# Kernel tuning notes

Hardware: AMD Instinct MI355X
Metric: run time of the kernel (lower is better)

Reference implementation:

```python
import jax, jax.numpy as jnp
import numpy as np

B, S, H = 1, 2048, 2048
QL, KVL = 1536, 512
NH, NOPE, ROPE, VD = 16, 128, 64, 128
IH, ID = 16, 128
TOPK = 512
EPS = 1e-6


def _rms_norm(x, g):
    return x * jax.lax.rsqrt(jnp.mean(x * x, -1, keepdims=True) + EPS) * g


def _layer_norm(x, g, b):
    m = jnp.mean(x, -1, keepdims=True)
    v = jnp.mean((x - m) ** 2, -1, keepdims=True)
    return (x - m) * jax.lax.rsqrt(v + EPS) * g + b


def _rope(x, cos, sin):
    # x: [B,S,h,D] (D even), cos/sin: [S,D//2]; neox-style rotate-halves
    x1, x2 = jnp.split(x, 2, -1)
    c = cos[None, :, None, :]
    s = sin[None, :, None, :]
    return jnp.concatenate([x1 * c - x2 * s, x1 * s + x2 * c], -1)


def setup_inputs() -> dict:
    key = jax.random.key(0)
    ks = jax.random.split(key, 10)
    rn = lambda k, sh: (jax.random.normal(k, sh) * 0.02).astype(jnp.float32)
    pos = jnp.arange(S, dtype=jnp.float32)
    inv = 1.0 / (10000.0 ** (jnp.arange(0, ROPE, 2, dtype=jnp.float32) / ROPE))
    ang = pos[:, None] * inv[None, :]  # [S, ROPE//2]
    return {
        "hidden_states": jax.random.normal(ks[0], (B, S, H), jnp.float32),
        "cos": jnp.cos(ang),
        "sin": jnp.sin(ang),
        "Wq_a": rn(ks[1], (H, QL)),
        "q_a_gamma": jnp.ones((QL,), jnp.float32),
        "Wq_b": rn(ks[2], (QL, NH * (NOPE + ROPE))),
        "Wkv_a": rn(ks[3], (H, KVL + ROPE)),
        "kv_a_gamma": jnp.ones((KVL,), jnp.float32),
        "Wkv_b": rn(ks[4], (KVL, NH * (NOPE + VD))),
        "Wo": rn(ks[5], (NH * VD, H)),
        "Wq_idx": rn(ks[6], (QL, IH * ID)),
        "Wk_idx": rn(ks[7], (H, ID)),
        "Ww_idx": rn(ks[8], (H, IH)),
        "kn_gamma": jnp.ones((ID,), jnp.float32),
        "kn_beta": jnp.zeros((ID,), jnp.float32),
        "topk": TOPK,
    }


def reference(hidden_states, cos, sin, Wq_a, q_a_gamma, Wq_b, Wkv_a, kv_a_gamma,
              Wkv_b, Wo, Wq_idx, Wk_idx, Ww_idx, kn_gamma, kn_beta, topk):
    b, s, _ = hidden_states.shape
    softmax_scale = (NOPE + ROPE) ** -0.5

    # ---- low-rank Q path ----
    q_a = _rms_norm(hidden_states @ Wq_a, q_a_gamma)                 # [B,S,QL]
    q = (q_a @ Wq_b).reshape(b, s, NH, NOPE + ROPE)
    q_nope, q_pe = q[..., :NOPE], _rope(q[..., NOPE:], cos, sin)

    # ---- latent KV path (MQA rope key) ----
    kv = hidden_states @ Wkv_a                                        # [B,S,KVL+ROPE]
    kv_c = _rms_norm(kv[..., :KVL], kv_a_gamma)
    k_pe = _rope(kv[..., KVL:][:, :, None, :], cos, sin)[:, :, 0]     # [B,S,ROPE]
    kvb = (kv_c @ Wkv_b).reshape(b, s, NH, NOPE + VD)
    k_nope, v = kvb[..., :NOPE], kvb[..., NOPE:]

    # ---- lightning indexer: I[t,s] = sum_h w[t,h] * relu(q_idx[t,h] . k_idx[s]) ----
    qi = (q_a @ Wq_idx).reshape(b, s, IH, ID)
    qi = jnp.concatenate([_rope(qi[..., :ROPE], cos, sin), qi[..., ROPE:]], -1)
    ki = _layer_norm(hidden_states @ Wk_idx, kn_gamma, kn_beta)       # [B,S,ID]
    ki = jnp.concatenate([_rope(ki[:, :, None, :ROPE], cos, sin)[:, :, 0], ki[..., ROPE:]], -1)
    w = hidden_states @ Ww_idx                                        # [B,S,IH]
    s_h = jax.nn.relu(jnp.einsum('bthd,bsd->bhts', qi, ki)) * (ID ** -0.5)
    idx_scores = jnp.einsum('bth,bhts->bts', w, s_h)                  # [B,S,S]

    causal = jnp.tril(jnp.ones((s, s), bool))
    idx_scores = jnp.where(causal[None], idx_scores, -jnp.inf)
    top_idx = jax.lax.top_k(idx_scores, topk)[1]                      # [B,S,topk]
    sel = jnp.zeros((b, s, s), bool).at[
        jnp.arange(b)[:, None, None], jnp.arange(s)[None, :, None], top_idx
    ].set(True)
    mask = sel & causal[None]                                         # [B,S,S]

    # ---- sparse MLA attention over selected tokens ----
    scores = (jnp.einsum('bthd,bshd->bhts', q_nope, k_nope)
              + jnp.einsum('bthd,bsd->bhts', q_pe, k_pe)) * softmax_scale
    scores = jnp.where(mask[:, None], scores, -jnp.inf)
    attn = jax.nn.softmax(scores, -1)                                 # [B,NH,S,S]
    out = jnp.einsum('bhts,bshd->bthd', attn, v).reshape(b, s, NH * VD)
    return out @ Wo                                                   # [B,S,H]
```

## Files before the change

kernel.cpp:

```cpp
#include <hip/hip_runtime.h>
#include <cstdint>
#include <cstddef>
#include <cmath>

typedef unsigned long long u64;
typedef __attribute__((ext_vector_type(8))) short bf16x8;
typedef __attribute__((ext_vector_type(4))) float f32x4;

static constexpr int S_    = 2048;
static constexpr int H_    = 2048;
static constexpr int TOPKC = 512;

#define SCALE_ATTN 0.07216878364870323f
#define ISCALE_ID  0.08838834764831845f
#define EPS_F 1e-6f

__device__ inline unsigned short f2b(float f) {
  unsigned u = __float_as_uint(f);
  return (unsigned short)((u + 0x7FFFu + ((u >> 16) & 1u)) >> 16);
}
__device__ inline float b2f(unsigned short b) {
  return __uint_as_float(((unsigned)b) << 16);
}
__device__ inline void gload16(const unsigned short* g, unsigned short* l) {
  __builtin_amdgcn_global_load_lds((const __attribute__((address_space(1))) void*)g,
                                   (__attribute__((address_space(3))) void*)l, 16, 0, 0);
}

__global__ __launch_bounds__(256) void k_gemm_bf16(
    const unsigned short* __restrict__ A, int lda,
    const unsigned short* __restrict__ Bt, int K,
    void* __restrict__ C, int ldc, int N, int out_bf16) {
  __shared__ unsigned short As[128 * 64];
  __shared__ unsigned short Bs[128 * 64];
  const int bm = blockIdx.y * 128, bn = blockIdx.x * 128;
  const int tid = threadIdx.x;
  const int lane = tid & 63, w = tid >> 6;
  const int wm = w >> 1, wn = w & 1;
  const int l15 = lane & 15, quarter = lane >> 4;
  const int srow = (lane >> 3), scol = (lane & 7) * 8;

  f32x4 acc[4][4];
#pragma unroll
  for (int i = 0; i < 4; i++)
#pragma unroll
    for (int j = 0; j < 4; j++) acc[i][j] = (f32x4){0.f, 0.f, 0.f, 0.f};

  for (int k0 = 0; k0 < K; k0 += 64) {
    __syncthreads();
#pragma unroll
    for (int i = 0; i < 4; i++) {
      int r0 = w * 32 + i * 8;
      gload16(A  + (size_t)(bm + r0 + srow) * lda + k0 + scol, &As[r0 * 64]);
      gload16(Bt + (size_t)(bn + r0 + srow) * K   + k0 + scol, &Bs[r0 * 64]);
    }
    __syncthreads();
#pragma unroll
    for (int kc = 0; kc < 2; kc++) {
      bf16x8 af[4], bfr[4];
#pragma unroll
      for (int mf = 0; mf < 4; mf++)
        af[mf] = *(const bf16x8*)(As + (wm * 64 + mf * 16 + l15) * 64 + kc * 32 + quarter * 8);
#pragma unroll
      for (int nf = 0; nf < 4; nf++)
        bfr[nf] = *(const bf16x8*)(Bs + (wn * 64 + nf * 16 + l15) * 64 + kc * 32 + quarter * 8);
#pragma unroll
      for (int mf = 0; mf < 4; mf++)
#pragma unroll
        for (int nf = 0; nf < 4; nf++)
          acc[mf][nf] = __builtin_amdgcn_mfma_f32_16x16x32_bf16(af[mf], bfr[nf], acc[mf][nf], 0, 0, 0);
    }
  }
#pragma unroll
  for (int mf = 0; mf < 4; mf++)
#pragma unroll
    for (int nf = 0; nf < 4; nf++)
#pragma unroll
      for (int r = 0; r < 4; r++) {
        int grow = bm + wm * 64 + mf * 16 + quarter * 4 + r;
        int gcol = bn + wn * 64 + nf * 16 + l15;
        if (gcol < N) {
          if (out_bf16) ((unsigned short*)C)[(size_t)grow * ldc + gcol] = f2b(acc[mf][nf][r]);
          else          ((float*)C)[(size_t)grow * ldc + gcol] = acc[mf][nf][r];
        }
      }
}

__device__ inline void tcast_tile(const float* __restrict__ W, int K, int N,
                                  unsigned short* __restrict__ dst,
                                  int r, int ntx, int tid, float (*T)[33]) {
  int xt = r % ntx, kt = r / ntx;
  int n0 = xt * 32, k0 = kt * 32;
#pragma unroll
  for (int i = 0; i < 4; i++) {
    int idx = tid + 256 * i;
    int rr = idx >> 5, c = idx & 31;
    T[rr][c] = W[(size_t)(k0 + rr) * N + n0 + c];
  }
  __syncthreads();
#pragma unroll
  for (int i = 0; i < 4; i++) {
    int idx = tid + 256 * i;
    int rr = idx >> 5, c = idx & 31;
    dst[(size_t)(n0 + rr) * K + k0 + c] = f2b(T[c][rr]);
  }
}

__global__ __launch_bounds__(256) void k_tcast_p1(
    const float* __restrict__ Wq_a, const float* __restrict__ Wkv_a,
    const float* __restrict__ Wk_idx, const float* __restrict__ Ww_idx,
    unsigned short* __restrict__ WT) {
  __shared__ float T[32][33];
  int bid = blockIdx.x, tid = threadIdx.x;
  if (bid < 3072)      tcast_tile(Wq_a,  2048, 1536, WT,                          bid,        48, tid, T);
  else if (bid < 4224) tcast_tile(Wkv_a, 2048,  576, WT + (size_t)1536 * 2048,    bid - 3072, 18, tid, T);
  else if (bid < 4480) tcast_tile(Wk_idx,2048,  128, WT + (size_t)2112 * 2048,    bid - 4224,  4, tid, T);
  else {
    int idx = (bid - 4480) * 256 + tid;
    int k = idx >> 4, n = idx & 15;
    WT[(size_t)(2240 + n) * 2048 + k] = f2b(Ww_idx[(size_t)k * 16 + n]);
  }
}

__global__ __launch_bounds__(256) void k_tcast_p2(
    const float* __restrict__ Wq_b, const float* __restrict__ Wq_idx,
    unsigned short* __restrict__ WT) {
  __shared__ float T[32][33];
  int bid = blockIdx.x, tid = threadIdx.x;
  if (bid < 4608) tcast_tile(Wq_b,   1536, 3072, WT,                        bid,        96, tid, T);
  else            tcast_tile(Wq_idx, 1536, 2048, WT + (size_t)3072 * 1536,  bid - 4608, 64, tid, T);
}

__global__ __launch_bounds__(256) void k_tcast_p3(
    const float* __restrict__ Wkv_b, const float* __restrict__ Wo,
    unsigned short* __restrict__ WT) {
  __shared__ float T[32][33];
  int bid = blockIdx.x, tid = threadIdx.x;
  if (bid < 2048) tcast_tile(Wkv_b,  512, 4096, WT,                       bid,        128, tid, T);
  else            tcast_tile(Wo,    2048, 2048, WT + (size_t)4096 * 512,  bid - 2048,  64, tid, T);
}

__global__ __launch_bounds__(256) void k_cast_bf16(const float* __restrict__ in, int pin,
                                                   unsigned short* __restrict__ outp, int pout,
                                                   int rows, int cols) {
  int cols4 = cols >> 2;
  int idx = blockIdx.x * 256 + threadIdx.x;
  if (idx >= rows * cols4) return;
  int r = idx / cols4, c = (idx - r * cols4) * 4;
  const float* ip = in + (size_t)r * pin + c;
  unsigned short* op = outp + (size_t)r * pout + c;
  op[0] = f2b(ip[0]); op[1] = f2b(ip[1]); op[2] = f2b(ip[2]); op[3] = f2b(ip[3]);
}

__global__ __launch_bounds__(256) void k_norms(
    const float* __restrict__ fat, int stride,
    const float* __restrict__ qg, const float* __restrict__ kvg,
    const float* __restrict__ kng, const float* __restrict__ knb,
    const float* __restrict__ cosb, const float* __restrict__ sinb,
    unsigned short* __restrict__ qa_b, unsigned short* __restrict__ kvc_b,
    unsigned short* __restrict__ kpe_b, unsigned short* __restrict__ ki_b) {
  int t = blockIdx.x, tid = threadIdx.x;
  const float* p = fat + (size_t)t * stride;
  __shared__ float red[256];
  __shared__ float buf[128];
  float x[6]; float s = 0.f;
#pragma unroll
  for (int i = 0; i < 6; i++) { x[i] = p[tid + 256 * i]; s += x[i] * x[i]; }
  red[tid] = s; __syncthreads();
  for (int st = 128; st > 0; st >>= 1) { if (tid < st) red[tid] += red[tid + st]; __syncthreads(); }
  float scl = rsqrtf(red[0] * (1.f / 1536.f) + EPS_F);
#pragma unroll
  for (int i = 0; i < 6; i++)
    qa_b[(size_t)t * 1536 + tid + 256 * i] = f2b(x[i] * scl * qg[tid + 256 * i]);
  __syncthreads();
  float y0 = p[1536 + tid], y1 = p[1792 + tid];
  red[tid] = y0 * y0 + y1 * y1; __syncthreads();
  for (int st = 128; st > 0; st >>= 1) { if (tid < st) red[tid] += red[tid + st]; __syncthreads(); }
  float scl2 = rsqrtf(red[0] * (1.f / 512.f) + EPS_F);
  kvc_b[(size_t)t * 512 + tid]       = f2b(y0 * scl2 * kvg[tid]);
  kvc_b[(size_t)t * 512 + 256 + tid] = f2b(y1 * scl2 * kvg[256 + tid]);
  if (tid < 32) {
    float a = p[2048 + tid], b = p[2080 + tid];
    float c = cosb[t * 32 + tid], sn = sinb[t * 32 + tid];
    kpe_b[(size_t)t * 64 + tid]      = f2b(a * c - b * sn);
    kpe_b[(size_t)t * 64 + 32 + tid] = f2b(a * sn + b * c);
  }
  __syncthreads();
  float z = (tid < 128) ? p[2112 + tid] : 0.f;
  red[tid] = z; __syncthreads();
  for (int st = 128; st > 0; st >>= 1) { if (tid < st) red[tid] += red[tid + st]; __syncthreads(); }
  float mean = red[0] * (1.f / 128.f);
  __syncthreads();
  float d = (tid < 128) ? (z - mean) : 0.f;
  red[tid] = d * d; __syncthreads();
  for (int st = 128; st > 0; st >>= 1) { if (tid < st) red[tid] += red[tid + st]; __syncthreads(); }
  float var = red[0] * (1.f / 128.f);
  if (tid < 128) buf[tid] = d * rsqrtf(var + EPS_F) * kng[tid] + knb[tid];
  __syncthreads();
  if (tid < 128) {
    float outv;
    if (tid < 32) {
      float c = cosb[t * 32 + tid], sn = sinb[t * 32 + tid];
      outv = buf[tid] * c - buf[tid + 32] * sn;
    } else if (tid < 64) {
      int j = tid - 32;
      float c = cosb[t * 32 + j], sn = sinb[t * 32 + j];
      outv = buf[j] * sn + buf[tid] * c;
    } else outv = buf[tid];
    ki_b[(size_t)t * 128 + tid] = f2b(outv);
  }
}

__global__ __launch_bounds__(256) void k_rope_b(unsigned short* __restrict__ base, int rowstride, int nh,
                                                int hstride, int off, const float* __restrict__ cosb,
                                                const float* __restrict__ sinb, int total) {
  int idx = blockIdx.x * 256 + threadIdx.x;
  if (idx >= total) return;
  int i = idx & 31, h = (idx >> 5) % nh, t = idx / (32 * nh);
  unsigned short* p = base + (size_t)t * rowstride + h * hstride + off;
  float x1 = b2f(p[i]), x2 = b2f(p[i + 32]);
  float c = cosb[t * 32 + i], s = sinb[t * 32 + i];
  p[i] = f2b(x1 * c - x2 * s);
  p[i + 32] = f2b(x1 * s + x2 * c);
}

__global__ __launch_bounds__(256) void k_idx_mfma(
    const unsigned short* __restrict__ qi_b, int qpitch,
    const unsigned short* __restrict__ ki_b,
    const float* __restrict__ wb, int wstride,
    float* __restrict__ out) {
  int bid = blockIdx.x;
  int tb = (int)((sqrtf(8.f * bid + 1.f) - 1.f) * 0.5f);
  while ((tb + 1) * (tb + 2) / 2 <= bid) tb++;
  while (tb * (tb + 1) / 2 > bid) tb--;
  int sb = bid - tb * (tb + 1) / 2;
  int t0 = tb * 64, s0 = sb * 64;

  int tid = threadIdx.x, lane = tid & 63, w = tid >> 6;
  int wm = w >> 1, wn = w & 1;
  int l15 = lane & 15, quarter = lane >> 4;

  __shared__ unsigned short Ks[64 * 128];
  __shared__ unsigned short Qs[2][64 * 128];
  __shared__ float Ws[64][16];

  int srow_[4], scc_[4];
#pragma unroll
  for (int i = 0; i < 4; i++) {
    int row = w * 16 + i * 4 + (lane >> 4);
    srow_[i] = row;
    scc_[i] = (lane & 15) ^ (row & 7);
  }
#pragma unroll
  for (int i = 0; i < 4; i++) {
    gload16(ki_b + (size_t)(s0 + srow_[i]) * 128 + scc_[i] * 8, &Ks[(w * 16 + i * 4) * 128]);
    gload16(qi_b + (size_t)(t0 + srow_[i]) * qpitch + scc_[i] * 8, &Qs[0][(w * 16 + i * 4) * 128]);
  }
  for (int i = tid; i < 64 * 16; i += 256) Ws[i >> 4][i & 15] = wb[(size_t)(t0 + (i >> 4)) * wstride + (i & 15)];
  __syncthreads();

  bf16x8 bfr[2][4];
#pragma unroll
  for (int nf = 0; nf < 2; nf++) {
    int row = wn * 32 + nf * 16 + l15;
    int rx = (row & 7) << 3;
#pragma unroll
    for (int kc = 0; kc < 4; kc++)
      bfr[nf][kc] = *(const bf16x8*)(Ks + row * 128 + ((kc * 32 + quarter * 8) ^ rx));
  }

  f32x4 acc[2][2];
#pragma unroll
  for (int mf = 0; mf < 2; mf++)
#pragma unroll
    for (int nf = 0; nf < 2; nf++) acc[mf][nf] = (f32x4){0.f, 0.f, 0.f, 0.f};

  for (int h = 0; h < 16; h++) {
    int cur = h & 1;
    if (h < 15) {
#pragma unroll
      for (int i = 0; i < 4; i++)
        gload16(qi_b + (size_t)(t0 + srow_[i]) * qpitch + (h + 1) * 128 + scc_[i] * 8,
                &Qs[cur ^ 1][(w * 16 + i * 4) * 128]);
    }
    f32x4 acch[2][2];
#pragma unroll
    for (int mf = 0; mf < 2; mf++)
#pragma unroll
      for (int nf = 0; nf < 2; nf++) acch[mf][nf] = (f32x4){0.f, 0.f, 0.f, 0.f};

    __builtin_amdgcn_s_setprio(1);
#pragma unroll
    for (int mf = 0; mf < 2; mf++) {
      int row = wm * 32 + mf * 16 + l15;
      int rx = (row & 7) << 3;
      bf16x8 af[4];
#pragma unroll
      for (int kc = 0; kc < 4; kc++)
        af[kc] = *(const bf16x8*)(Qs[cur] + row * 128 + ((kc * 32 + quarter * 8) ^ rx));
#pragma unroll
      for (int nf = 0; nf < 2; nf++)
#pragma unroll
        for (int kc = 0; kc < 4; kc++)
          acch[mf][nf] = __builtin_amdgcn_mfma_f32_16x16x32_bf16(af[kc], bfr[nf][kc], acch[mf][nf], 0, 0, 0);
    }
    __builtin_amdgcn_s_setprio(0);
#pragma unroll
    for (int mf = 0; mf < 2; mf++) {
#pragma unroll
      for (int r = 0; r < 4; r++) {
        float wv = Ws[wm * 32 + mf * 16 + quarter * 4 + r][h];
#pragma unroll
        for (int nf = 0; nf < 2; nf++)
          acc[mf][nf][r] = fmaf(wv, fmaxf(acch[mf][nf][r], 0.f), acc[mf][nf][r]);
      }
    }
    __syncthreads();
  }
#pragma unroll
  for (int mf = 0; mf < 2; mf++)
#pragma unroll
    for (int nf = 0; nf < 2; nf++)
#pragma unroll
      for (int r = 0; r < 4; r++) {
        int t = t0 + wm * 32 + mf * 16 + quarter * 4 + r;
        int s = s0 + wn * 32 + nf * 16 + l15;
        out[(size_t)t * 2048 + s] = acc[mf][nf][r] * ISCALE_ID;
      }
}

__global__ __launch_bounds__(256) void k_topk_mask(const float* __restrict__ idx_sc, u64* __restrict__ maskw) {
  int t = blockIdx.x;
  int tid = threadIdx.x;
  int n = t + 1;
  if (n <= TOPKC) {
    if (tid < 32) {
      int lo = tid * 64, hi = lo + 63;
      u64 wv;
      if (t >= hi) wv = ~0ULL;
      else if (t < lo) wv = 0ULL;
      else wv = (~0ULL) >> (63 - (t - lo));
      maskw[(size_t)t * 32 + tid] = wv;
    }
    return;
  }
  __shared__ unsigned int u[2048];
  __shared__ int hist[256];
  __shared__ int scan[256];
  __shared__ u64 mw[32];
  __shared__ int sel_b, new_target, tie_base;
  __shared__ int wcnt[4];
  if (tid < 32) mw[tid] = 0ULL;
  const float* row = idx_sc + (size_t)t * 2048;
  for (int s = tid; s < n; s += 256) {
    unsigned int bb = __float_as_uint(row[s]);
    u[s] = (bb & 0x80000000u) ? ~bb : (bb | 0x80000000u);
  }
  __syncthreads();
  unsigned int prefix = 0;
  int target = TOPKC;
  for (int shift = 24; shift >= 0; shift -= 8) {
    hist[tid] = 0;
    __syncthreads();
    unsigned int himask = (shift == 24) ? 0u : (0xFFFFFFFFu << (shift + 8));
    for (int s = tid; s < n; s += 256) {
      unsigned int uv = u[s];
      if ((uv & himask) == prefix) atomicAdd(&hist[(uv >> shift) & 0xFF], 1);
    }
    __syncthreads();
    scan[tid] = hist[tid];
    __syncthreads();
#pragma unroll
    for (int st = 1; st < 256; st <<= 1) {
      int add = (tid + st < 256) ? scan[tid + st] : 0;
      __syncthreads();
      scan[tid] += add;
      __syncthreads();
    }
    int snext = (tid == 255) ? 0 : scan[tid + 1];
    if (scan[tid] >= target && snext < target) { sel_b = tid; new_target = target - snext; }
    __syncthreads();
    prefix |= ((unsigned int)sel_b) << shift;
    target = new_target;
    __syncthreads();
  }
  if (tid == 0) tie_base = 0;
  __syncthreads();
  int wid = tid >> 6, lane = tid & 63;
  for (int s0 = 0; s0 < n; s0 += 256) {
    int s = s0 + tid;
    bool in = (s < n);
    unsigned int uv = in ? u[s] : 0u;
    bool gt = in && (uv > prefix);
    bool tie = in && (uv == prefix);
    u64 bal = __ballot(tie);
    if (lane == 0) wcnt[wid] = __popcll(bal);
    __syncthreads();
    int wbase = tie_base;
    for (int wI = 0; wI < wid; wI++) wbase += wcnt[wI];
    int rank = wbase + __popcll(bal & ((1ULL << lane) - 1ULL));
    bool sel = gt || (tie && rank < target);
    if (sel) atomicOr(&mw[s >> 6], 1ULL << (s & 63));
    __syncthreads();
    if (tid == 0) tie_base += wcnt[0] + wcnt[1] + wcnt[2] + wcnt[3];
    __syncthreads();
  }
  if (tid < 32) maskw[(size_t)t * 32 + tid] = mw[tid];
}

__global__ __launch_bounds__(256) void k_attn_mfma(
    const unsigned short* __restrict__ qb, int qpitch,
    const unsigned short* __restrict__ kvb_b,
    const unsigned short* __restrict__ kpe_b,
    const float* __restrict__ cosb, const float* __restrict__ sinb,
    const u64* __restrict__ maskw,
    unsigned short* __restrict__ opart,
    float* __restrict__ mlbuf) {
  int ybm = blockIdx.x;
  int h = blockIdx.y;
  int ph = blockIdx.z;
  int yb = (h < 8) ? ybm : (31 - ybm);
  int t0 = yb * 64;
  int tid = threadIdx.x;
  int lane = tid & 63, wq = tid >> 6;
  int quarter = lane >> 4, l15 = lane & 15;

  __shared__ unsigned short Kd[2][32 * 192];
  __shared__ unsigned short Vts[128 * 32];

  const unsigned short* kb_base[3];
  int kb_step[3];
#pragma unroll
  for (int i = 0; i < 3; i++) {
    int slot = (wq * 3 + i) * 1024 + lane * 16;
    int rowk = slot / 384;
    int coff = slot - rowk * 384;
    int cc = (coff ^ ((rowk & 7) << 4)) >> 4;
    if (cc < 16) { kb_base[i] = kvb_b + (size_t)rowk * 4096 + h * 256 + cc * 8; kb_step[i] = 4096; }
    else         { kb_base[i] = kpe_b + (size_t)rowk * 64 + (cc - 16) * 8;      kb_step[i] = 64; }
  }
  const int vdg = tid & 15, vsp = tid >> 4;
  const unsigned short* vbase = kvb_b + (size_t)(vsp * 2) * 4096 + h * 256 + 128 + vdg * 8;

  bf16x8 qf[6];
  {
    int t = t0 + wq * 16 + l15;
    const unsigned short* qp = qb + (size_t)t * qpitch + h * 192 + quarter * 8;
#pragma unroll
    for (int kc = 0; kc < 6; kc++) qf[kc] = *(const bf16x8*)(qp + kc * 32);
    const float* cp = cosb + t * 32 + quarter * 8;
    const float* sp = sinb + t * 32 + quarter * 8;
    float4 ca = *(const float4*)cp,  cb2 = *(const float4*)(cp + 4);
    float4 sa = *(const float4*)sp,  sb2 = *(const float4*)(sp + 4);
    float carr[8] = {ca.x, ca.y, ca.z, ca.w, cb2.x, cb2.y, cb2.z, cb2.w};
    float sarr[8] = {sa.x, sa.y, sa.z, sa.w, sb2.x, sb2.y, sb2.z, sb2.w};
#pragma unroll
    for (int j = 0; j < 8; j++) {
      float x1 = b2f((unsigned short)qf[4][j]);
      float x2 = b2f((unsigned short)qf[5][j]);
      qf[4][j] = (short)f2b(x1 * carr[j] - x2 * sarr[j]);
      qf[5][j] = (short)f2b(x1 * sarr[j] + x2 * carr[j]);
    }
  }

  f32x4 o[8];
#pragma unroll
  for (int df = 0; df < 8; df++) o[df] = (f32x4){0.f, 0.f, 0.f, 0.f};
  float mcol = -__builtin_inff(), lcol = 0.f;
  const u64* mrow = maskw + (size_t)(t0 + wq * 16 + l15) * 32;
  int ntile = 2 * yb + 2;

  {
    size_t sr = (size_t)ph * 32;
#pragma unroll
    for (int i = 0; i < 3; i++) gload16(kb_base[i] + sr * kb_step[i], &Kd[0][(wq * 3 + i) * 512]);
  }
  bf16x8 vr0 = *(const bf16x8*)(vbase + (size_t)ph * 32 * 4096);
  bf16x8 vr1 = *(const bf16x8*)(vbase + (size_t)(ph * 32 + 1) * 4096);
  __syncthreads();
#pragma unroll
  for (int j = 0; j < 8; j++) {
    int d = vdg * 8 + j;
    unsigned pack = (unsigned)(unsigned short)vr0[j] | (((unsigned)(unsigned short)vr1[j]) << 16);
    *(unsigned*)((char*)Vts + d * 64 + ((vsp * 4) ^ ((d & 3) << 4))) = pack;
  }

  int cur = 0;
  for (int k = ph; k < ntile; k += 2) {
    __syncthreads();
    bool pf = (k + 2 < ntile);
    if (pf) {
      size_t sn = (size_t)(k + 2) * 32;
#pragma unroll
      for (int i = 0; i < 3; i++)
        gload16(kb_base[i] + sn * kb_step[i], &Kd[cur ^ 1][(wq * 3 + i) * 512]);
      const unsigned short* vp = vbase + sn * 4096;
      vr0 = *(const bf16x8*)vp;
      vr1 = *(const bf16x8*)(vp + 4096);
    }
    int s0 = k * 32;
    const unsigned short* Kc = Kd[cur];
    f32x4 sfT[2];
    __builtin_amdgcn_s_setprio(1);
#pragma unroll
    for (int sc = 0; sc < 2; sc++) {
      f32x4 a = (f32x4){0.f, 0.f, 0.f, 0.f};
      int row = sc * 16 + l15;
      int rx = (row & 7) << 4;
#pragma unroll
      for (int kc = 0; kc < 6; kc++) {
        int byte = row * 384 + ((kc * 64 + quarter * 16) ^ rx);
        bf16x8 kf = *(const bf16x8*)((const char*)Kc + byte);
        a = __builtin_amdgcn_mfma_f32_16x16x32_bf16(kf, qf[kc], a, 0, 0, 0);
      }
      sfT[sc] = a;
    }
    __builtin_amdgcn_s_setprio(0);
    u64 w64 = mrow[s0 >> 6];
    int shiftb = s0 & 32;
    float p[2][4];
#pragma unroll
    for (int sc = 0; sc < 2; sc++)
#pragma unroll
      for (int r = 0; r < 4; r++) {
        int sbit = shiftb + sc * 16 + quarter * 4 + r;
        bool sel = (w64 >> sbit) & 1ULL;
        p[sc][r] = sel ? sfT[sc][r] * SCALE_ATTN : -__builtin_inff();
      }
    float v = p[0][0];
    v = fmaxf(v, p[0][1]); v = fmaxf(v, p[0][2]); v = fmaxf(v, p[0][3]);
    v = fmaxf(v, p[1][0]); v = fmaxf(v, p[1][1]); v = fmaxf(v, p[1][2]); v = fmaxf(v, p[1][3]);
    v = fmaxf(v, __shfl_xor(v, 16));
    v = fmaxf(v, __shfl_xor(v, 32));
    bool need = __any(v > mcol + 8.f);
    float scl = 1.f;
    if (need) {
      float mn = fmaxf(mcol, v);
      bool dead = (mn == -__builtin_inff());
      scl = dead ? 1.f : __expf(mcol - mn);
#pragma unroll
      for (int sc = 0; sc < 2; sc++)
#pragma unroll
        for (int r = 0; r < 4; r++)
          p[sc][r] = dead ? 0.f : __expf(p[sc][r] - mn);
      mcol = dead ? mcol : mn;
    } else {
      float basem = (mcol == -__builtin_inff()) ? 0.f : mcol;
#pragma unroll
      for (int sc = 0; sc < 2; sc++)
#pragma unroll
        for (int r = 0; r < 4; r++)
          p[sc][r] = __expf(p[sc][r] - basem);
    }
    float rs = p[0][0] + p[0][1] + p[0][2] + p[0][3] + p[1][0] + p[1][1] + p[1][2] + p[1][3];
    rs += __shfl_xor(rs, 16);
    rs += __shfl_xor(rs, 32);
    lcol = lcol * scl + rs;

    unsigned pk0[2], pk1[2];
#pragma unroll
    for (int rr = 0; rr < 2; rr++) {
      pk0[rr] = (unsigned)f2b(p[0][2 * rr]) | (((unsigned)f2b(p[0][2 * rr + 1])) << 16);
      pk1[rr] = (unsigned)f2b(p[1][2 * rr]) | (((unsigned)f2b(p[1][2 * rr + 1])) << 16);
    }
    union { unsigned d[4]; bf16x8 v; } pu;
#pragma unroll
    for (int jj = 0; jj < 4; jj++) {
      int src = ((quarter & 1) * 2 + (jj >> 1)) * 16 + l15;
      unsigned a0 = (unsigned)__shfl((int)pk0[jj & 1], src);
      unsigned a1 = (unsigned)__shfl((int)pk1[jj & 1], src);
      pu.d[jj] = (quarter < 2) ? a0 : a1;
    }
    bf16x8 pa = pu.v;

    if (need) {
      float sclr[4];
#pragma unroll
      for (int r = 0; r < 4; r++) sclr[r] = __shfl(scl, quarter * 4 + r);
#pragma unroll
      for (int df = 0; df < 8; df++)
#pragma unroll
        for (int r = 0; r < 4; r++) o[df][r] *= sclr[r];
    }
    __builtin_amdgcn_s_setprio(1);
#pragma unroll
    for (int df = 0; df < 8; df++) {
      int d = df * 16 + l15;
      int vbyte = d * 64 + ((quarter * 16) ^ ((d & 3) << 4));
      bf16x8 vf = *(const bf16x8*)((const char*)Vts + vbyte);
      o[df] = __builtin_amdgcn_mfma_f32_16x16x32_bf16(pa, vf, o[df], 0, 0, 0);
    }
    __builtin_amdgcn_s_setprio(0);
    __syncthreads();
    if (pf) {
#pragma unroll
      for (int j = 0; j < 8; j++) {
        int d = vdg * 8 + j;
        unsigned pack = (unsigned)(unsigned short)vr0[j] | (((unsigned)(unsigned short)vr1[j]) << 16);
        *(unsigned*)((char*)Vts + d * 64 + ((vsp * 4) ^ ((d & 3) << 4))) = pack;
      }
    }
    cur ^= 1;
  }
  unsigned short* ob = opart + (size_t)ph * S_ * 2048;
#pragma unroll
  for (int r = 0; r < 4; r++) {
    int t = t0 + wq * 16 + quarter * 4 + r;
    unsigned short* op = ob + (size_t)t * 2048 + h * 128 + l15;
#pragma unroll
    for (int df = 0; df < 8; df++) op[df * 16] = f2b(o[df][r]);
  }
  if (quarter == 0) {
    int t = t0 + wq * 16 + l15;
    float* mp = mlbuf + ((size_t)ph * S_ * 16 + (size_t)t * 16 + h) * 2;
    mp[0] = mcol;
    mp[1] = lcol;
  }
}

__global__ __launch_bounds__(256) void k_attn_merge(
    const unsigned short* __restrict__ opart, const float* __restrict__ mlbuf,
    unsigned short* __restrict__ attn_b) {
  int idx = blockIdx.x * 256 + threadIdx.x;
  int dg = idx & 15, h = (idx >> 4) & 15, t = idx >> 8;
  const float* ml0 = mlbuf + ((size_t)t * 16 + h) * 2;
  const float* ml1 = ml0 + (size_t)S_ * 16 * 2;
  float m0 = ml0[0], l0 = ml0[1];
  float m1 = ml1[0], l1 = ml1[1];
  float m = fmaxf(m0, m1);
  float w0 = (m0 == -__builtin_inff()) ? 0.f : __expf(m0 - m);
  float w1 = (m1 == -__builtin_inff()) ? 0.f : __expf(m1 - m);
  float L = l0 * w0 + l1 * w1;
  float inv = (L > 0.f) ? 1.f / L : 0.f;
  const bf16x8 o0 = *(const bf16x8*)(opart + (size_t)t * 2048 + h * 128 + dg * 8);
  const bf16x8 o1 = *(const bf16x8*)(opart + (size_t)S_ * 2048 + (size_t)t * 2048 + h * 128 + dg * 8);
  bf16x8 r;
#pragma unroll
  for (int j = 0; j < 8; j++) {
    float a = b2f((unsigned short)o0[j]) * w0 + b2f((unsigned short)o1[j]) * w1;
    r[j] = (short)f2b(a * inv);
  }
  *(bf16x8*)(attn_b + (size_t)t * 2048 + h * 128 + dg * 8) = r;
}

extern "C" void kernel_launch(void* const* d_in, const int* in_sizes, int n_in,
                              void* d_out, int out_size, void* d_ws, size_t ws_size,
                              hipStream_t stream) {
  const float* hs     = (const float*)d_in[0];
  const float* cosb   = (const float*)d_in[1];
  const float* sinb   = (const float*)d_in[2];
  const float* Wq_a   = (const float*)d_in[3];
  const float* q_a_g  = (const float*)d_in[4];
  const float* Wq_b   = (const float*)d_in[5];
  const float* Wkv_a  = (const float*)d_in[6];
  const float* kv_a_g = (const float*)d_in[7];
  const float* Wkv_b  = (const float*)d_in[8];
  const float* Wo     = (const float*)d_in[9];
  const float* Wq_idx = (const float*)d_in[10];
  const float* Wk_idx = (const float*)d_in[11];
  const float* Ww_idx = (const float*)d_in[12];
  const float* kn_g   = (const float*)d_in[13];
  const float* kn_b   = (const float*)d_in[14];
  float* out = (float*)d_out;

  char* base = (char*)d_ws;
  size_t off = 0;
  auto alloc = [&](size_t bytes) { void* p = base + off; off += (bytes + 255) & ~size_t(255); return p; };

  float* fat1 = (float*)alloc((size_t)S_ * 2304 * 4);
  unsigned short* attn_b = (unsigned short*)fat1;
  float* idxs = (float*)alloc((size_t)S_ * 2048 * 4);
  unsigned short* opart = (unsigned short*)idxs;
  unsigned short* fat2 = (unsigned short*)alloc((size_t)S_ * 5120 * 2);
  float* mlbuf = (float*)alloc((size_t)2 * S_ * 16 * 2 * 4);
  u64*   maskw = (u64*)alloc((size_t)S_ * 32 * 8);
  unsigned short* hs_b  = (unsigned short*)alloc((size_t)S_ * 2048 * 2);
  unsigned short* qa_b  = (unsigned short*)alloc((size_t)S_ * 1536 * 2);
  unsigned short* kvc_b = (unsigned short*)alloc((size_t)S_ * 512 * 2);
  unsigned short* kpe_b = (unsigned short*)alloc((size_t)S_ * 64 * 2);
  unsigned short* kvb_b = (unsigned short*)alloc((size_t)S_ * 4096 * 2);
  unsigned short* ki_b  = (unsigned short*)alloc((size_t)S_ * 128 * 2);
  unsigned short* WT    = (unsigned short*)alloc((size_t)5120 * 1536 * 2);

  dim3 blk(256);

  k_cast_bf16<<<dim3((S_ * 2048 / 4) / 256), blk, 0, stream>>>(hs, 2048, hs_b, 2048, S_, 2048);
  k_tcast_p1<<<dim3(4608), blk, 0, stream>>>(Wq_a, Wkv_a, Wk_idx, Ww_idx, WT);
  k_gemm_bf16<<<dim3(18, 16), blk, 0, stream>>>(hs_b, 2048, WT, 2048, fat1, 2304, 2256, 0);
  k_norms<<<dim3(S_), blk, 0, stream>>>(fat1, 2304, q_a_g, kv_a_g, kn_g, kn_b, cosb, sinb,
                                        qa_b, kvc_b, kpe_b, ki_b);
  k_tcast_p2<<<dim3(7680), blk, 0, stream>>>(Wq_b, Wq_idx, WT);
  k_gemm_bf16<<<dim3(40, 16), blk, 0, stream>>>(qa_b, 1536, WT, 1536, fat2, 5120, 5120, 1);
  k_rope_b<<<dim3((S_ * 16 * 32) / 256), blk, 0, stream>>>(fat2 + 3072, 5120, 16, 128, 0, cosb, sinb, S_ * 16 * 32);
  k_tcast_p3<<<dim3(6144), blk, 0, stream>>>(Wkv_b, Wo, WT);
  k_gemm_bf16<<<dim3(32, 16), blk, 0, stream>>>(kvc_b, 512, WT, 512, kvb_b, 4096, 4096, 1);
  k_idx_mfma<<<dim3(528), blk, 0, stream>>>(fat2 + 3072, 5120, ki_b, fat1 + 2240, 2304, idxs);
  k_topk_mask<<<dim3(S_), blk, 0, stream>>>(idxs, maskw);
  k_attn_mfma<<<dim3(32, 16, 2), blk, 0, stream>>>(fat2, 5120, kvb_b, kpe_b, cosb, sinb, maskw,
                                                   opart, mlbuf);
  k_attn_merge<<<dim3((S_ * 16 * 16) / 256), blk, 0, stream>>>(opart, mlbuf, attn_b);
  k_gemm_bf16<<<dim3(16, 16), blk, 0, stream>>>(attn_b, 2048, WT + (size_t)4096 * 512, 2048, out, 2048, 2048, 0);

  (void)in_sizes; (void)n_in; (void)out_size; (void)ws_size;
}
```

Before: 380.4 us.

## Split only long causal query tiles across two blocks, use 64-key tiles

The attention kernel now splits the key range into two halves only for the 16 longest query tiles (second half of the sequence). Short tiles are processed whole by one block, which normalizes its output and writes it directly. Key/value tiles grow from 32 to 64 keys per iteration, which doubles shared memory use and the number of MFMAs per step. The merge kernel now only handles the split rows. The aim is to cut merge traffic and per-iteration overhead while keeping load balance, at the cost of fewer blocks (768 vs 1024) and higher LDS use that may lower occupancy.

```diff
diff --git a/kernel.cpp b/kernel.cpp
--- a/kernel.cpp
+++ b/kernel.cpp
@@ -414,25 +414,37 @@
     const unsigned short* __restrict__ kpe_b,
     const float* __restrict__ cosb, const float* __restrict__ sinb,
     const u64* __restrict__ maskw,
+    unsigned short* __restrict__ attn_b,
     unsigned short* __restrict__ opart,
     float* __restrict__ mlbuf) {
-  int ybm = blockIdx.x;
-  int h = blockIdx.y;
-  int ph = blockIdx.z;
-  int yb = (h < 8) ? ybm : (31 - ybm);
+  int b = blockIdx.x, h = blockIdx.y;
+  int yb, k0, k1, half = 0;
+  bool partial;
+  if (b < 32) {
+    yb = 31 - (b >> 1);
+    int n = yb + 1, h1 = (n + 1) >> 1;
+    half = b & 1;
+    partial = true;
+    k0 = half ? h1 : 0;
+    k1 = half ? n : h1;
+  } else {
+    yb = 47 - b;
+    k0 = 0; k1 = yb + 1;
+    partial = false;
+  }
   int t0 = yb * 64;
   int tid = threadIdx.x;
   int lane = tid & 63, wq = tid >> 6;
   int quarter = lane >> 4, l15 = lane & 15;
 
-  __shared__ unsigned short Kd[2][32 * 192];
-  __shared__ unsigned short Vts[128 * 32];
-
-  const unsigned short* kb_base[3];
-  int kb_step[3];
-#pragma unroll
-  for (int i = 0; i < 3; i++) {
-    int slot = (wq * 3 + i) * 1024 + lane * 16;
+  __shared__ unsigned short Kd[2][64 * 192];
+  __shared__ unsigned short Vts[128 * 64];
+
+  const unsigned short* kb_base[6];
+  int kb_step[6];
+#pragma unroll
+  for (int i = 0; i < 6; i++) {
+    int slot = (wq * 6 + i) * 1024 + lane * 16;
     int rowk = slot / 384;
     int coff = slot - rowk * 384;
     int cc = (coff ^ ((rowk & 7) << 4)) >> 4;
@@ -440,7 +452,7 @@
     else         { kb_base[i] = kpe_b + (size_t)rowk * 64 + (cc - 16) * 8;      kb_step[i] = 64; }
   }
   const int vdg = tid & 15, vsp = tid >> 4;
-  const unsigned short* vbase = kvb_b + (size_t)(vsp * 2) * 4096 + h * 256 + 128 + vdg * 8;
+  const unsigned short* vbase = kvb_b + (size_t)(vsp * 4) * 4096 + h * 256 + 128 + vdg * 8;
 
   bf16x8 qf[6];
   {
@@ -468,42 +480,44 @@
   for (int df = 0; df < 8; df++) o[df] = (f32x4){0.f, 0.f, 0.f, 0.f};
   float mcol = -__builtin_inff(), lcol = 0.f;
   const u64* mrow = maskw + (size_t)(t0 + wq * 16 + l15) * 32;
-  int ntile = 2 * yb + 2;
-
-  {
-    size_t sr = (size_t)ph * 32;
-#pragma unroll
-    for (int i = 0; i < 3; i++) gload16(kb_base[i] + sr * kb_step[i], &Kd[0][(wq * 3 + i) * 512]);
-  }
-  bf16x8 vr0 = *(const bf16x8*)(vbase + (size_t)ph * 32 * 4096);
-  bf16x8 vr1 = *(const bf16x8*)(vbase + (size_t)(ph * 32 + 1) * 4096);
+
+#pragma unroll
+  for (int i = 0; i < 6; i++)
+    gload16(kb_base[i] + (size_t)(k0 * 64) * kb_step[i], &Kd[0][(wq * 6 + i) * 512]);
+  bf16x8 vr0 = *(const bf16x8*)(vbase + (size_t)(k0 * 64) * 4096);
+  bf16x8 vr1 = *(const bf16x8*)(vbase + (size_t)(k0 * 64 + 1) * 4096);
+  bf16x8 vr2 = *(const bf16x8*)(vbase + (size_t)(k0 * 64 + 2) * 4096);
+  bf16x8 vr3 = *(const bf16x8*)(vbase + (size_t)(k0 * 64 + 3) * 4096);
   __syncthreads();
 #pragma unroll
   for (int j = 0; j < 8; j++) {
     int d = vdg * 8 + j;
-    unsigned pack = (unsigned)(unsigned short)vr0[j] | (((unsigned)(unsigned short)vr1[j]) << 16);
-    *(unsigned*)((char*)Vts + d * 64 + ((vsp * 4) ^ ((d & 3) << 4))) = pack;
+    uint2 w2;
+    w2.x = (unsigned)(unsigned short)vr0[j] | (((unsigned)(unsigned short)vr1[j]) << 16);
+    w2.y = (unsigned)(unsigned short)vr2[j] | (((unsigned)(unsigned short)vr3[j]) << 16);
+    *(uint2*)((char*)Vts + d * 128 + ((vsp * 8) ^ (((d >> 2) & 7) << 4))) = w2;
   }
 
   int cur = 0;
-  for (int k = ph; k < ntile; k += 2) {
-    __syncthreads();
-    bool pf = (k + 2 < ntile);
+  for (int k = k0; k < k1; k++, cur ^= 1) {
+    __syncthreads();
+    bool pf = (k + 1 < k1);
     if (pf) {
-      size_t sn = (size_t)(k + 2) * 32;
-#pragma unroll
-      for (int i = 0; i < 3; i++)
-        gload16(kb_base[i] + sn * kb_step[i], &Kd[cur ^ 1][(wq * 3 + i) * 512]);
+      size_t sn = (size_t)(k + 1) * 64;
+#pragma unroll
+      for (int i = 0; i < 6; i++)
+        gload16(kb_base[i] + sn * kb_step[i], &Kd[cur ^ 1][(wq * 6 + i) * 512]);
       const unsigned short* vp = vbase + sn * 4096;
-      vr0 = *(const bf16x8*)vp;
+      vr0 = *(const bf16x8*)(vp);
       vr1 = *(const bf16x8*)(vp + 4096);
-    }
-    int s0 = k * 32;
+      vr2 = *(const bf16x8*)(vp + 8192);
+      vr3 = *(const bf16x8*)(vp + 12288);
+    }
     const unsigned short* Kc = Kd[cur];
-    f32x4 sfT[2];
+    f32x4 sfT[4];
     __builtin_amdgcn_s_setprio(1);
 #pragma unroll
-    for (int sc = 0; sc < 2; sc++) {
+    for (int sc = 0; sc < 4; sc++) {
       f32x4 a = (f32x4){0.f, 0.f, 0.f, 0.f};
       int row = sc * 16 + l15;
       int rx = (row & 7) << 4;
@@ -516,20 +530,21 @@
       sfT[sc] = a;
     }
     __builtin_amdgcn_s_setprio(0);
-    u64 w64 = mrow[s0 >> 6];
-    int shiftb = s0 & 32;
-    float p[2][4];
-#pragma unroll
-    for (int sc = 0; sc < 2; sc++)
+    u64 w64 = mrow[k];
+    float p[4][4];
+#pragma unroll
+    for (int sc = 0; sc < 4; sc++)
 #pragma unroll
       for (int r = 0; r < 4; r++) {
-        int sbit = shiftb + sc * 16 + quarter * 4 + r;
+        int sbit = sc * 16 + quarter * 4 + r;
         bool sel = (w64 >> sbit) & 1ULL;
         p[sc][r] = sel ? sfT[sc][r] * SCALE_ATTN : -__builtin_inff();
       }
     float v = p[0][0];
-    v = fmaxf(v, p[0][1]); v = fmaxf(v, p[0][2]); v = fmaxf(v, p[0][3]);
-    v = fmaxf(v, p[1][0]); v = fmaxf(v, p[1][1]); v = fmaxf(v, p[1][2]); v = fmaxf(v, p[1][3]);
+#pragma unroll
+    for (int sc = 0; sc < 4; sc++)
+#pragma unroll
+      for (int r = 0; r < 4; r++) v = fmaxf(v, p[sc][r]);
     v = fmaxf(v, __shfl_xor(v, 16));
     v = fmaxf(v, __shfl_xor(v, 32));
     bool need = __any(v > mcol + 8.f);
@@ -539,7 +554,7 @@
       bool dead = (mn == -__builtin_inff());
       scl = dead ? 1.f : __expf(mcol - mn);
 #pragma unroll
-      for (int sc = 0; sc < 2; sc++)
+      for (int sc = 0; sc < 4; sc++)
 #pragma unroll
         for (int r = 0; r < 4; r++)
           p[sc][r] = dead ? 0.f : __expf(p[sc][r] - mn);
@@ -547,32 +562,39 @@
     } else {
       float basem = (mcol == -__builtin_inff()) ? 0.f : mcol;
 #pragma unroll
-      for (int sc = 0; sc < 2; sc++)
+      for (int sc = 0; sc < 4; sc++)
 #pragma unroll
         for (int r = 0; r < 4; r++)
           p[sc][r] = __expf(p[sc][r] - basem);
     }
-    float rs = p[0][0] + p[0][1] + p[0][2] + p[0][3] + p[1][0] + p[1][1] + p[1][2] + p[1][3];
+    float rs = 0.f;
+#pragma unroll
+    for (int sc = 0; sc < 4; sc++)
+#pragma unroll
+      for (int r = 0; r < 4; r++) rs += p[sc][r];
     rs += __shfl_xor(rs, 16);
     rs += __shfl_xor(rs, 32);
     lcol = lcol * scl + rs;
 
-    unsigned pk0[2], pk1[2];
-#pragma unroll
-    for (int rr = 0; rr < 2; rr++) {
-      pk0[rr] = (unsigned)f2b(p[0][2 * rr]) | (((unsigned)f2b(p[0][2 * rr + 1])) << 16);
-      pk1[rr] = (unsigned)f2b(p[1][2 * rr]) | (((unsigned)f2b(p[1][2 * rr + 1])) << 16);
-    }
-    union { unsigned d[4]; bf16x8 v; } pu;
-#pragma unroll
-    for (int jj = 0; jj < 4; jj++) {
-      int src = ((quarter & 1) * 2 + (jj >> 1)) * 16 + l15;
-      unsigned a0 = (unsigned)__shfl((int)pk0[jj & 1], src);
-      unsigned a1 = (unsigned)__shfl((int)pk1[jj & 1], src);
-      pu.d[jj] = (quarter < 2) ? a0 : a1;
-    }
-    bf16x8 pa = pu.v;
-
+    unsigned pk[4][2];
+#pragma unroll
+    for (int sc = 0; sc < 4; sc++)
+#pragma unroll
+      for (int rr = 0; rr < 2; rr++)
+        pk[sc][rr] = (unsigned)f2b(p[sc][2 * rr]) | (((unsigned)f2b(p[sc][2 * rr + 1])) << 16);
+    bf16x8 pa[2];
+#pragma unroll
+    for (int kc = 0; kc < 2; kc++) {
+      union { unsigned d[4]; bf16x8 v; } pu;
+#pragma unroll
+      for (int jj = 0; jj < 4; jj++) {
+        int src = ((quarter & 1) * 2 + (jj >> 1)) * 16 + l15;
+        unsigned lo = (unsigned)__shfl((int)pk[kc * 2][jj & 1], src);
+        unsigned hi = (unsigned)__shfl((int)pk[kc * 2 + 1][jj & 1], src);
+        pu.d[jj] = (quarter < 2) ? lo : hi;
+      }
+      pa[kc] = pu.v;
+    }
     if (need) {
       float sclr[4];
 #pragma unroll
@@ -584,37 +606,55 @@
     }
     __builtin_amdgcn_s_setprio(1);
 #pragma unroll
-    for (int df = 0; df < 8; df++) {
-      int d = df * 16 + l15;
-      int vbyte = d * 64 + ((quarter * 16) ^ ((d & 3) << 4));
-      bf16x8 vf = *(const bf16x8*)((const char*)Vts + vbyte);
-      o[df] = __builtin_amdgcn_mfma_f32_16x16x32_bf16(pa, vf, o[df], 0, 0, 0);
-    }
+    for (int kc = 0; kc < 2; kc++)
+#pragma unroll
+      for (int df = 0; df < 8; df++) {
+        int d = df * 16 + l15;
+        int vbyte = d * 128 + ((kc * 64 + quarter * 16) ^ (((d >> 2) & 7) << 4));
+        bf16x8 vf = *(const bf16x8*)((const char*)Vts + vbyte);
+        o[df] = __builtin_amdgcn_mfma_f32_16x16x32_bf16(pa[kc], vf, o[df], 0, 0, 0);
+      }
     __builtin_amdgcn_s_setprio(0);
     __syncthreads();
     if (pf) {
 #pragma unroll
       for (int j = 0; j < 8; j++) {
         int d = vdg * 8 + j;
-        unsigned pack = (unsigned)(unsigned short)vr0[j] | (((unsigned)(unsigned short)vr1[j]) << 16);
-        *(unsigned*)((char*)Vts + d * 64 + ((vsp * 4) ^ ((d & 3) << 4))) = pack;
+        uint2 w2;
+        w2.x = (unsigned)(unsigned short)vr0[j] | (((unsigned)(unsigned short)vr1[j]) << 16);
+        w2.y = (unsigned)(unsigned short)vr2[j] | (((unsigned)(unsigned short)vr3[j]) << 16);
+        *(uint2*)((char*)Vts + d * 128 + ((vsp * 8) ^ (((d >> 2) & 7) << 4))) = w2;
       }
     }
-    cur ^= 1;
-  }
-  unsigned short* ob = opart + (size_t)ph * S_ * 2048;
-#pragma unroll
-  for (int r = 0; r < 4; r++) {
-    int t = t0 + wq * 16 + quarter * 4 + r;
-    unsigned short* op = ob + (size_t)t * 2048 + h * 128 + l15;
-#pragma unroll
-    for (int df = 0; df < 8; df++) op[df * 16] = f2b(o[df][r]);
-  }
-  if (quarter == 0) {
-    int t = t0 + wq * 16 + l15;
-    float* mp = mlbuf + ((size_t)ph * S_ * 16 + (size_t)t * 16 + h) * 2;
-    mp[0] = mcol;
-    mp[1] = lcol;
+  }
+
+  if (!partial) {
+    float inv = (lcol > 0.f) ? 1.f / lcol : 0.f;
+    float invr[4];
+#pragma unroll
+    for (int r = 0; r < 4; r++) invr[r] = __shfl(inv, quarter * 4 + r);
+#pragma unroll
+    for (int r = 0; r < 4; r++) {
+      int t = t0 + wq * 16 + quarter * 4 + r;
+      unsigned short* op = attn_b + (size_t)t * 2048 + h * 128 + l15;
+#pragma unroll
+      for (int df = 0; df < 8; df++) op[df * 16] = f2b(o[df][r] * invr[r]);
+    }
+  } else {
+    unsigned short* ob = opart + (size_t)half * 1024 * 2048;
+#pragma unroll
+    for (int r = 0; r < 4; r++) {
+      int t = t0 + wq * 16 + quarter * 4 + r;
+      unsigned short* op = ob + (size_t)(t - 1024) * 2048 + h * 128 + l15;
+#pragma unroll
+      for (int df = 0; df < 8; df++) op[df * 16] = f2b(o[df][r]);
+    }
+    if (quarter == 0) {
+      int t = t0 + wq * 16 + l15;
+      float* mp = mlbuf + (((size_t)half * 1024 + (t - 1024)) * 16 + h) * 2;
+      mp[0] = mcol;
+      mp[1] = lcol;
+    }
   }
 }
 
@@ -622,9 +662,10 @@
     const unsigned short* __restrict__ opart, const float* __restrict__ mlbuf,
     unsigned short* __restrict__ attn_b) {
   int idx = blockIdx.x * 256 + threadIdx.x;
-  int dg = idx & 15, h = (idx >> 4) & 15, t = idx >> 8;
-  const float* ml0 = mlbuf + ((size_t)t * 16 + h) * 2;
-  const float* ml1 = ml0 + (size_t)S_ * 16 * 2;
+  int dg = idx & 15, h = (idx >> 4) & 15, tr = idx >> 8;
+  int t = 1024 + tr;
+  const float* ml0 = mlbuf + ((size_t)tr * 16 + h) * 2;
+  const float* ml1 = ml0 + (size_t)1024 * 16 * 2;
   float m0 = ml0[0], l0 = ml0[1];
   float m1 = ml1[0], l1 = ml1[1];
   float m = fmaxf(m0, m1);
@@ -632,8 +673,8 @@
   float w1 = (m1 == -__builtin_inff()) ? 0.f : __expf(m1 - m);
   float L = l0 * w0 + l1 * w1;
   float inv = (L > 0.f) ? 1.f / L : 0.f;
-  const bf16x8 o0 = *(const bf16x8*)(opart + (size_t)t * 2048 + h * 128 + dg * 8);
-  const bf16x8 o1 = *(const bf16x8*)(opart + (size_t)S_ * 2048 + (size_t)t * 2048 + h * 128 + dg * 8);
+  const bf16x8 o0 = *(const bf16x8*)(opart + (size_t)tr * 2048 + h * 128 + dg * 8);
+  const bf16x8 o1 = *(const bf16x8*)(opart + (size_t)1024 * 2048 + (size_t)tr * 2048 + h * 128 + dg * 8);
   bf16x8 r;
 #pragma unroll
   for (int j = 0; j < 8; j++) {
@@ -672,7 +713,7 @@
   float* idxs = (float*)alloc((size_t)S_ * 2048 * 4);
   unsigned short* opart = (unsigned short*)idxs;
   unsigned short* fat2 = (unsigned short*)alloc((size_t)S_ * 5120 * 2);
-  float* mlbuf = (float*)alloc((size_t)2 * S_ * 16 * 2 * 4);
+  float* mlbuf = (float*)alloc((size_t)2 * 1024 * 16 * 2 * 4);
   u64*   maskw = (u64*)alloc((size_t)S_ * 32 * 8);
   unsigned short* hs_b  = (unsigned short*)alloc((size_t)S_ * 2048 * 2);
   unsigned short* qa_b  = (unsigned short*)alloc((size_t)S_ * 1536 * 2);
@@ -696,9 +737,9 @@
   k_gemm_bf16<<<dim3(32, 16), blk, 0, stream>>>(kvc_b, 512, WT, 512, kvb_b, 4096, 4096, 1);
   k_idx_mfma<<<dim3(528), blk, 0, stream>>>(fat2 + 3072, 5120, ki_b, fat1 + 2240, 2304, idxs);
   k_topk_mask<<<dim3(S_), blk, 0, stream>>>(idxs, maskw);
-  k_attn_mfma<<<dim3(32, 16, 2), blk, 0, stream>>>(fat2, 5120, kvb_b, kpe_b, cosb, sinb, maskw,
-                                                   opart, mlbuf);
-  k_attn_merge<<<dim3((S_ * 16 * 16) / 256), blk, 0, stream>>>(opart, mlbuf, attn_b);
+  k_attn_mfma<<<dim3(48, 16), blk, 0, stream>>>(fat2, 5120, kvb_b, kpe_b, cosb, sinb, maskw,
+                                                attn_b, opart, mlbuf);
+  k_attn_merge<<<dim3((1024 * 16 * 16) / 256), blk, 0, stream>>>(opart, mlbuf, attn_b);
   k_gemm_bf16<<<dim3(16, 16), blk, 0, stream>>>(attn_b, 2048, WT + (size_t)4096 * 512, 2048, out, 2048, 2048, 0);
 
   (void)in_sizes; (void)n_in; (void)out_size; (void)ws_size;
```

After: 370.7 us. -2.5%, faster.
